# Performance work log

Measured on AMD Instinct MI355X. Metric: run time of the kernel, lower is better.

The kernel has to match this reference:

```python
import jax, jax.numpy as jnp
import numpy as np
from jax import lax

WIN_SIZE = 11
WIN_SIGMA = 1.5
DATA_RANGE = 1.0
K1, K2 = 0.01, 0.03


def _gauss_1d(win_size, sigma):
    coords = jnp.arange(win_size, dtype=jnp.float32) - win_size // 2
    g = jnp.exp(-(coords ** 2) / (2.0 * sigma ** 2))
    return g / jnp.sum(g)


def _gauss_filter(x, win):
    # Separable depthwise gaussian blur, VALID padding (matches pytorch_msssim).
    C = x.shape[1]
    kh = jnp.tile(win.reshape(1, 1, -1, 1), (C, 1, 1, 1))  # (C,1,k,1)
    kw = jnp.tile(win.reshape(1, 1, 1, -1), (C, 1, 1, 1))  # (C,1,1,k)
    dn = ('NCHW', 'OIHW', 'NCHW')
    x = lax.conv_general_dilated(x, kh, (1, 1), 'VALID',
                                 dimension_numbers=dn, feature_group_count=C)
    x = lax.conv_general_dilated(x, kw, (1, 1), 'VALID',
                                 dimension_numbers=dn, feature_group_count=C)
    return x


def _ssim(X, Y, win, data_range):
    C1 = (K1 * data_range) ** 2
    C2 = (K2 * data_range) ** 2
    mu1 = _gauss_filter(X, win)
    mu2 = _gauss_filter(Y, win)
    mu1_sq = mu1 * mu1
    mu2_sq = mu2 * mu2
    mu1_mu2 = mu1 * mu2
    sigma1_sq = _gauss_filter(X * X, win) - mu1_sq
    sigma2_sq = _gauss_filter(Y * Y, win) - mu2_sq
    sigma12 = _gauss_filter(X * Y, win) - mu1_mu2
    cs_map = (2.0 * sigma12 + C2) / (sigma1_sq + sigma2_sq + C2)
    ssim_map = ((2.0 * mu1_mu2 + C1) / (mu1_sq + mu2_sq + C1)) * cs_map
    return jnp.mean(ssim_map)


def setup_inputs() -> dict:
    key = jax.random.key(0)
    k1, k2 = jax.random.split(key)
    shape = (16, 3, 384, 512)
    pred = jax.random.uniform(k1, shape, dtype=jnp.float32)
    target = jax.random.uniform(k2, shape, dtype=jnp.float32)
    return {"pred": pred, "target": target}


def reference(pred, target):
    win = _gauss_1d(WIN_SIZE, WIN_SIGMA)
    ssim_val = _ssim(pred, target, win, DATA_RANGE)
    return 1.0 - ssim_val
```

## Files before the change

### kernel.cpp

```cpp
#include <hip/hip_runtime.h>
#include <math.h>

#define WIN 11
#define IMG_H 384
#define IMG_W 512
#define OUT_H (IMG_H - WIN + 1)
#define OUT_W (IMG_W - WIN + 1)
#define RPW 2
#define NPAIRS (OUT_H / RPW)
#define NIMG 48
#define NBLOCKS (NPAIRS * NIMG)
#define BLOCKS_PER_XCD (NBLOCKS / 8)
#define NBUCKETS 256

struct GaussW { float g[WIN]; };

__device__ __forceinline__ void horiz11(const float (&acc)[8], float (&out)[8],
                                        int lane, const GaussW& gw)
{
    float v[18];
    #pragma unroll
    for (int j = 0; j < 8; ++j) v[j] = acc[j];
    #pragma unroll
    for (int j = 0; j < 8; ++j) v[8 + j] = __shfl(acc[j], lane + 1, 64);
    v[16] = __shfl(acc[0], lane + 2, 64);
    v[17] = __shfl(acc[1], lane + 2, 64);
    #pragma unroll
    for (int j = 0; j < 8; ++j) {
        float o = 0.f;
        #pragma unroll
        for (int k = 0; k < WIN; ++k) o = fmaf(gw.g[k], v[j + k], o);
        out[j] = o;
    }
}

__device__ __forceinline__ float row_ssim(float (&acc)[5][8], int lane, int c0,
                                          const GaussW& gw)
{
    float h[5][8];
    #pragma unroll
    for (int ch = 0; ch < 5; ++ch) horiz11(acc[ch], h[ch], lane, gw);
    const float C1 = 1e-4f, C2 = 9e-4f;
    float s = 0.f;
    #pragma unroll
    for (int j = 0; j < 8; ++j) {
        float mu1 = h[0][j], mu2 = h[1][j];
        float mu1s = mu1 * mu1, mu2s = mu2 * mu2, m12 = mu1 * mu2;
        float s1  = h[2][j] - mu1s;
        float s2  = h[3][j] - mu2s;
        float s12 = h[4][j] - m12;
        float num = fmaf(2.f, m12, C1) * fmaf(2.f, s12, C2);
        float den = (mu1s + mu2s + C1) * (s1 + s2 + C2);
        float ssim = num * __builtin_amdgcn_rcpf(den);
        s += (c0 + j < OUT_W) ? ssim : 0.f;
    }
    return s;
}

__global__ __launch_bounds__(64, 4) void ssim_fused_kernel(
    const float* __restrict__ X, const float* __restrict__ Y,
    double* __restrict__ accum, GaussW gw)
{
    const int lane = threadIdx.x & 63;

    const int id   = blockIdx.x;
    const int wid  = (id & 7) * BLOCKS_PER_XCD + (id >> 3);
    const int img  = wid / NPAIRS;
    const int pair = wid % NPAIRS;
    const int r0   = pair * RPW;
    const int c0 = lane << 3;
    const float* __restrict__ Xb = X + ((size_t)img * IMG_H + r0) * IMG_W + c0;
    const float* __restrict__ Yb = Y + ((size_t)img * IMG_H + r0) * IMG_W + c0;

    float a[RPW][5][8];
    #pragma unroll
    for (int r = 0; r < RPW; ++r)
        #pragma unroll
        for (int ch = 0; ch < 5; ++ch)
            #pragma unroll
            for (int j = 0; j < 8; ++j) a[r][ch][j] = 0.f;

    #pragma unroll
    for (int k = 0; k < RPW + WIN - 1; ++k) {
        const float* rx = Xb + (size_t)k * IMG_W;
        const float* ry = Yb + (size_t)k * IMG_W;
        float4 xa = *(const float4*)(rx);
        float4 xb = *(const float4*)(rx + 4);
        float4 ya = *(const float4*)(ry);
        float4 yb = *(const float4*)(ry + 4);
        float xs[8] = {xa.x, xa.y, xa.z, xa.w, xb.x, xb.y, xb.z, xb.w};
        float ys[8] = {ya.x, ya.y, ya.z, ya.w, yb.x, yb.y, yb.z, yb.w};
        #pragma unroll
        for (int r = 0; r < RPW; ++r) {
            if (k - r >= 0 && k - r < WIN) {
                const float g = gw.g[k - r];
                #pragma unroll
                for (int j = 0; j < 8; ++j) {
                    float x = xs[j], y = ys[j];
                    a[r][0][j] = fmaf(g, x, a[r][0][j]);
                    a[r][1][j] = fmaf(g, y, a[r][1][j]);
                    float t = g * x;
                    a[r][2][j] = fmaf(t, x, a[r][2][j]);
                    a[r][4][j] = fmaf(t, y, a[r][4][j]);
                    float u = g * y;
                    a[r][3][j] = fmaf(u, y, a[r][3][j]);
                }
            }
        }
    }

    float sum = row_ssim(a[0], lane, c0, gw) + row_ssim(a[1], lane, c0, gw);

    #pragma unroll
    for (int off = 32; off; off >>= 1)
        sum += __shfl_down(sum, off, 64);
    if (lane == 0)
        atomicAdd(&accum[id & (NBUCKETS - 1)], (double)sum);
}

__global__ void ssim_finalize_kernel(const double* __restrict__ accum,
                                     float* __restrict__ out, double inv_count)
{
    const int lane = threadIdx.x;
    double s = 0.0;
    for (int i = lane; i < NBUCKETS; i += 64) s += accum[i];
    #pragma unroll
    for (int off = 32; off; off >>= 1)
        s += __shfl_down(s, off, 64);
    if (lane == 0) out[0] = (float)(1.0 - s * inv_count);
}

extern "C" void kernel_launch(void* const* d_in, const int* in_sizes, int n_in,
                              void* d_out, int out_size, void* d_ws, size_t ws_size,
                              hipStream_t stream) {
    const float* X = (const float*)d_in[0];
    const float* Y = (const float*)d_in[1];
    float* out = (float*)d_out;
    double* accum = (double*)d_ws;

    GaussW gw;
    {
        double g[WIN], ssum = 0.0;
        for (int i = 0; i < WIN; ++i) {
            double d = (double)i - WIN / 2;
            g[i] = exp(-(d * d) / (2.0 * 1.5 * 1.5));
            ssum += g[i];
        }
        for (int i = 0; i < WIN; ++i) gw.g[i] = (float)(g[i] / ssum);
    }

    hipMemsetAsync(accum, 0, NBUCKETS * sizeof(double), stream);

    ssim_fused_kernel<<<NBLOCKS, 64, 0, stream>>>(X, Y, accum, gw);

    const double inv_count = 1.0 / ((double)(NIMG) * OUT_H * OUT_W);
    ssim_finalize_kernel<<<1, 64, 0, stream>>>(accum, out, inv_count);
}
```

Baseline: 133.0 us.

## Use packed float2 FMAs, 4-wave blocks, and per-block slots instead of atomics

Accumulators and the horizontal Gaussian pass are recast as two-wide float vectors so the compiler can emit packed FP32 FMA instructions. The horizontal pass pairs odd taps with a shifted packed layout. Blocks now hold 4 waves covering 8 output rows, reduced through shared memory. Each block writes one double slot instead of a bucketed atomic add, which removes the memset. The finalize kernel sums all slots with 256 threads. This aims to halve VALU instruction count and cut launch and atomic overhead, at the cost of extra register shuffling, a block barrier and some idle waves in the final band.

```diff
diff --git a/kernel.cpp b/kernel.cpp
--- a/kernel.cpp
+++ b/kernel.cpp
@@ -7,127 +7,162 @@
 #define OUT_H (IMG_H - WIN + 1)
 #define OUT_W (IMG_W - WIN + 1)
 #define RPW 2
-#define NPAIRS (OUT_H / RPW)
+#define WPB 4
+#define ROWS_PER_BLOCK (RPW * WPB)
+#define BANDS ((OUT_H + ROWS_PER_BLOCK - 1) / ROWS_PER_BLOCK)
 #define NIMG 48
-#define NBLOCKS (NPAIRS * NIMG)
-#define BLOCKS_PER_XCD (NBLOCKS / 8)
-#define NBUCKETS 256
+#define NBLOCKS (BANDS * NIMG)
+#define BPX (NBLOCKS / 8)
+
+typedef float v2 __attribute__((ext_vector_type(2)));
 
 struct GaussW { float g[WIN]; };
 
-__device__ __forceinline__ void horiz11(const float (&acc)[8], float (&out)[8],
-                                        int lane, const GaussW& gw)
+__device__ __forceinline__ void horiz11_pk(const v2 (&acc)[4], v2 (&out)[4],
+                                           int lane, const GaussW& gw)
 {
-    float v[18];
+    v2 P[9];
     #pragma unroll
-    for (int j = 0; j < 8; ++j) v[j] = acc[j];
+    for (int q = 0; q < 4; ++q) P[q] = acc[q];
     #pragma unroll
-    for (int j = 0; j < 8; ++j) v[8 + j] = __shfl(acc[j], lane + 1, 64);
-    v[16] = __shfl(acc[0], lane + 2, 64);
-    v[17] = __shfl(acc[1], lane + 2, 64);
+    for (int q = 0; q < 4; ++q) {
+        P[4 + q].x = __shfl(acc[q].x, lane + 1, 64);
+        P[4 + q].y = __shfl(acc[q].y, lane + 1, 64);
+    }
+    P[8].x = __shfl(acc[0].x, lane + 2, 64);
+    P[8].y = __shfl(acc[0].y, lane + 2, 64);
+    v2 O[8];
     #pragma unroll
-    for (int j = 0; j < 8; ++j) {
-        float o = 0.f;
+    for (int p = 0; p < 8; ++p) { O[p].x = P[p].y; O[p].y = P[p + 1].x; }
+    #pragma unroll
+    for (int q = 0; q < 4; ++q) {
+        v2 o = 0.f;
         #pragma unroll
-        for (int k = 0; k < WIN; ++k) o = fmaf(gw.g[k], v[j + k], o);
-        out[j] = o;
+        for (int m = 0; m < 6; ++m) {
+            v2 gg = gw.g[2 * m];
+            o = __builtin_elementwise_fma(gg, P[q + m], o);
+        }
+        #pragma unroll
+        for (int m = 0; m < 5; ++m) {
+            v2 gg = gw.g[2 * m + 1];
+            o = __builtin_elementwise_fma(gg, O[q + m], o);
+        }
+        out[q] = o;
     }
 }
 
-__device__ __forceinline__ float row_ssim(float (&acc)[5][8], int lane, int c0,
-                                          const GaussW& gw)
+__device__ __forceinline__ float row_ssim_pk(v2 (&A)[5][4], int lane, int c0,
+                                             const GaussW& gw)
 {
-    float h[5][8];
+    v2 h[5][4];
     #pragma unroll
-    for (int ch = 0; ch < 5; ++ch) horiz11(acc[ch], h[ch], lane, gw);
-    const float C1 = 1e-4f, C2 = 9e-4f;
+    for (int ch = 0; ch < 5; ++ch) horiz11_pk(A[ch], h[ch], lane, gw);
+    const v2 C1 = 1e-4f, C2 = 9e-4f, two = 2.f;
     float s = 0.f;
     #pragma unroll
-    for (int j = 0; j < 8; ++j) {
-        float mu1 = h[0][j], mu2 = h[1][j];
-        float mu1s = mu1 * mu1, mu2s = mu2 * mu2, m12 = mu1 * mu2;
-        float s1  = h[2][j] - mu1s;
-        float s2  = h[3][j] - mu2s;
-        float s12 = h[4][j] - m12;
-        float num = fmaf(2.f, m12, C1) * fmaf(2.f, s12, C2);
-        float den = (mu1s + mu2s + C1) * (s1 + s2 + C2);
-        float ssim = num * __builtin_amdgcn_rcpf(den);
-        s += (c0 + j < OUT_W) ? ssim : 0.f;
+    for (int q = 0; q < 4; ++q) {
+        v2 mu1 = h[0][q], mu2 = h[1][q];
+        v2 mu1s = mu1 * mu1, mu2s = mu2 * mu2, m12 = mu1 * mu2;
+        v2 s1  = h[2][q] - mu1s;
+        v2 s2  = h[3][q] - mu2s;
+        v2 s12 = h[4][q] - m12;
+        v2 num = __builtin_elementwise_fma(two, m12, C1) *
+                 __builtin_elementwise_fma(two, s12, C2);
+        v2 den = (mu1s + mu2s + C1) * (s1 + s2 + C2);
+        float r0 = num.x * __builtin_amdgcn_rcpf(den.x);
+        float r1 = num.y * __builtin_amdgcn_rcpf(den.y);
+        int c = c0 + 2 * q;
+        s += (c < OUT_W) ? r0 : 0.f;
+        s += (c + 1 < OUT_W) ? r1 : 0.f;
     }
     return s;
 }
 
-__global__ __launch_bounds__(64, 4) void ssim_fused_kernel(
+__global__ __launch_bounds__(256, 4) void ssim_fused_kernel(
     const float* __restrict__ X, const float* __restrict__ Y,
-    double* __restrict__ accum, GaussW gw)
+    double* __restrict__ slots, GaussW gw)
 {
-    const int lane = threadIdx.x & 63;
+    const int tid  = threadIdx.x;
+    const int wave = tid >> 6;
+    const int lane = tid & 63;
 
     const int id   = blockIdx.x;
-    const int wid  = (id & 7) * BLOCKS_PER_XCD + (id >> 3);
-    const int img  = wid / NPAIRS;
-    const int pair = wid % NPAIRS;
-    const int r0   = pair * RPW;
+    const int wid  = (id & 7) * BPX + (id >> 3);
+    const int img  = wid / BANDS;
+    const int band = wid % BANDS;
+    const int r0   = band * ROWS_PER_BLOCK + wave * RPW;
+
     const int c0 = lane << 3;
-    const float* __restrict__ Xb = X + ((size_t)img * IMG_H + r0) * IMG_W + c0;
-    const float* __restrict__ Yb = Y + ((size_t)img * IMG_H + r0) * IMG_W + c0;
+    float sum = 0.f;
 
-    float a[RPW][5][8];
-    #pragma unroll
-    for (int r = 0; r < RPW; ++r)
+    if (r0 < OUT_H) {
+        const float* __restrict__ Xb = X + ((size_t)img * IMG_H + r0) * IMG_W + c0;
+        const float* __restrict__ Yb = Y + ((size_t)img * IMG_H + r0) * IMG_W + c0;
+
+        v2 A[RPW][5][4];
         #pragma unroll
-        for (int ch = 0; ch < 5; ++ch)
+        for (int r = 0; r < RPW; ++r)
             #pragma unroll
-            for (int j = 0; j < 8; ++j) a[r][ch][j] = 0.f;
+            for (int ch = 0; ch < 5; ++ch)
+                #pragma unroll
+                for (int q = 0; q < 4; ++q) A[r][ch][q] = 0.f;
 
-    #pragma unroll
-    for (int k = 0; k < RPW + WIN - 1; ++k) {
-        const float* rx = Xb + (size_t)k * IMG_W;
-        const float* ry = Yb + (size_t)k * IMG_W;
-        float4 xa = *(const float4*)(rx);
-        float4 xb = *(const float4*)(rx + 4);
-        float4 ya = *(const float4*)(ry);
-        float4 yb = *(const float4*)(ry + 4);
-        float xs[8] = {xa.x, xa.y, xa.z, xa.w, xb.x, xb.y, xb.z, xb.w};
-        float ys[8] = {ya.x, ya.y, ya.z, ya.w, yb.x, yb.y, yb.z, yb.w};
         #pragma unroll
-        for (int r = 0; r < RPW; ++r) {
-            if (k - r >= 0 && k - r < WIN) {
-                const float g = gw.g[k - r];
-                #pragma unroll
-                for (int j = 0; j < 8; ++j) {
-                    float x = xs[j], y = ys[j];
-                    a[r][0][j] = fmaf(g, x, a[r][0][j]);
-                    a[r][1][j] = fmaf(g, y, a[r][1][j]);
-                    float t = g * x;
-                    a[r][2][j] = fmaf(t, x, a[r][2][j]);
-                    a[r][4][j] = fmaf(t, y, a[r][4][j]);
-                    float u = g * y;
-                    a[r][3][j] = fmaf(u, y, a[r][3][j]);
+        for (int k = 0; k < RPW + WIN - 1; ++k) {
+            const float* rx = Xb + (size_t)k * IMG_W;
+            const float* ry = Yb + (size_t)k * IMG_W;
+            float4 xa = *(const float4*)(rx);
+            float4 xb = *(const float4*)(rx + 4);
+            float4 ya = *(const float4*)(ry);
+            float4 yb = *(const float4*)(ry + 4);
+            v2 xs[4] = {{xa.x, xa.y}, {xa.z, xa.w}, {xb.x, xb.y}, {xb.z, xb.w}};
+            v2 ys[4] = {{ya.x, ya.y}, {ya.z, ya.w}, {yb.x, yb.y}, {yb.z, yb.w}};
+            #pragma unroll
+            for (int r = 0; r < RPW; ++r) {
+                if (k - r >= 0 && k - r < WIN) {
+                    v2 g = gw.g[k - r];
+                    #pragma unroll
+                    for (int q = 0; q < 4; ++q) {
+                        v2 x = xs[q], y = ys[q];
+                        A[r][0][q] = __builtin_elementwise_fma(g, x, A[r][0][q]);
+                        A[r][1][q] = __builtin_elementwise_fma(g, y, A[r][1][q]);
+                        v2 t = g * x;
+                        A[r][2][q] = __builtin_elementwise_fma(t, x, A[r][2][q]);
+                        A[r][4][q] = __builtin_elementwise_fma(t, y, A[r][4][q]);
+                        v2 u = g * y;
+                        A[r][3][q] = __builtin_elementwise_fma(u, y, A[r][3][q]);
+                    }
                 }
             }
         }
+
+        sum = row_ssim_pk(A[0], lane, c0, gw) + row_ssim_pk(A[1], lane, c0, gw);
+
+        #pragma unroll
+        for (int off = 32; off; off >>= 1)
+            sum += __shfl_down(sum, off, 64);
     }
 
-    float sum = row_ssim(a[0], lane, c0, gw) + row_ssim(a[1], lane, c0, gw);
-
-    #pragma unroll
-    for (int off = 32; off; off >>= 1)
-        sum += __shfl_down(sum, off, 64);
-    if (lane == 0)
-        atomicAdd(&accum[id & (NBUCKETS - 1)], (double)sum);
+    __shared__ float ws[WPB];
+    if (lane == 0) ws[wave] = sum;
+    __syncthreads();
+    if (tid == 0)
+        slots[id] = (double)(ws[0] + ws[1] + ws[2] + ws[3]);
 }
 
-__global__ void ssim_finalize_kernel(const double* __restrict__ accum,
+__global__ void ssim_finalize_kernel(const double* __restrict__ slots,
                                      float* __restrict__ out, double inv_count)
 {
-    const int lane = threadIdx.x;
+    const int t = threadIdx.x;
     double s = 0.0;
-    for (int i = lane; i < NBUCKETS; i += 64) s += accum[i];
+    for (int i = t; i < NBLOCKS; i += 256) s += slots[i];
     #pragma unroll
     for (int off = 32; off; off >>= 1)
         s += __shfl_down(s, off, 64);
-    if (lane == 0) out[0] = (float)(1.0 - s * inv_count);
+    __shared__ double w[4];
+    if ((t & 63) == 0) w[t >> 6] = s;
+    __syncthreads();
+    if (t == 0) out[0] = (float)(1.0 - (w[0] + w[1] + w[2] + w[3]) * inv_count);
 }
 
 extern "C" void kernel_launch(void* const* d_in, const int* in_sizes, int n_in,
@@ -136,7 +171,7 @@
     const float* X = (const float*)d_in[0];
     const float* Y = (const float*)d_in[1];
     float* out = (float*)d_out;
-    double* accum = (double*)d_ws;
+    double* slots = (double*)d_ws;
 
     GaussW gw;
     {
@@ -149,10 +184,8 @@
         for (int i = 0; i < WIN; ++i) gw.g[i] = (float)(g[i] / ssum);
     }
 
-    hipMemsetAsync(accum, 0, NBUCKETS * sizeof(double), stream);
+    ssim_fused_kernel<<<NBLOCKS, 256, 0, stream>>>(X, Y, slots, gw);
 
-    ssim_fused_kernel<<<NBLOCKS, 64, 0, stream>>>(X, Y, accum, gw);
-
-    const double inv_count = 1.0 / ((double)(NIMG) * OUT_H * OUT_W);
-    ssim_finalize_kernel<<<1, 64, 0, stream>>>(accum, out, inv_count);
+    const double inv_count = 1.0 / ((double)NIMG * OUT_H * OUT_W);
+    ssim_finalize_kernel<<<1, 256, 0, stream>>>(slots, out, inv_count);
 }
```

New measurement: 162.8 us. 1.22x slower.
